# Kernel tuning notes

Hardware: AMD Instinct MI355X
Metric: run time of the kernel (lower is better)

The kernel has to match this reference:

```python
import jax, jax.numpy as jnp
import numpy as np

N, H, B = 500000, 256, 512  # nodes, hidden_dim, number of graphs


def setup_inputs() -> dict:
    key = jax.random.key(0)
    k1, k2, k3, k4 = jax.random.split(key, 4)
    x = jax.random.normal(k1, (N, H), dtype=jnp.float32)
    batch = jnp.sort(jax.random.randint(k2, (N,), 0, B)).astype(jnp.int64)
    # attention_pool params (Linear(H,H) -> Tanh -> Linear(H,1))
    s1 = 1.0 / np.sqrt(H)
    W1 = jax.random.uniform(k3, (H, H), jnp.float32, -s1, s1)
    b1 = jnp.zeros((H,), jnp.float32)
    W2 = jax.random.uniform(k4, (H, 1), jnp.float32, -s1, s1)
    b2 = jnp.zeros((1,), jnp.float32)
    return {"x": x, "batch": batch, "W1": W1, "b1": b1, "W2": W2, "b2": b2}


def reference(x, batch, W1, b1, W2, b2):
    # attention scores per node: Linear -> tanh -> Linear -> scalar
    s = (jnp.tanh(x @ W1 + b1) @ W2 + b2)[:, 0]            # [N]
    # segment-wise softmax over nodes of each graph (numerically stable)
    seg_max = jax.ops.segment_max(s, batch, num_segments=B)  # [B]
    e = jnp.exp(s - seg_max[batch])                          # [N]
    denom = jax.ops.segment_sum(e, batch, num_segments=B)    # [B]
    w = e / denom[batch]                                     # [N]
    attn_pool = jax.ops.segment_sum(x * w[:, None], batch, num_segments=B)  # [B,H]
    # mean pool
    sums = jax.ops.segment_sum(x, batch, num_segments=B)     # [B,H]
    counts = jax.ops.segment_sum(jnp.ones((x.shape[0],), x.dtype), batch, num_segments=B)
    mean_pool = sums / jnp.maximum(counts, 1.0)[:, None]
    # max pool (guard empty segments -> 0, matching zero-init buffer behavior)
    max_pool = jax.ops.segment_max(x, batch, num_segments=B)
    max_pool = jnp.where(counts[:, None] > 0, max_pool, 0.0)
    return jnp.concatenate([mean_pool, max_pool, attn_pool], axis=1)  # [B, 3H]
```

## Files before the change

### kernel.cpp

```cpp
#include <hip/hip_runtime.h>

#define HDIM 256
#define MTILE 64
#define NITER 4
#define APITCH 264
#define PROWS 256
#define CHUNK 16

typedef __attribute__((ext_vector_type(8))) short short8;
typedef __attribute__((ext_vector_type(4))) short short4v;
typedef __attribute__((ext_vector_type(4))) float floatx4;

__device__ __forceinline__ unsigned short f2bf(float f){
  unsigned u = __float_as_uint(f);
  u += 0x7FFFu + ((u>>16)&1u);
  return (unsigned short)(u>>16);
}
__device__ __forceinline__ unsigned fkey(float f){
  unsigned u = __float_as_uint(f);
  return u ^ ((unsigned)((int)u>>31) | 0x80000000u);
}
__device__ __forceinline__ float fdec(unsigned u){
  unsigned b = (u & 0x80000000u) ? (u & 0x7FFFFFFFu) : ~u;
  return __uint_as_float(b);
}

__global__ void k_zero(float* __restrict__ p, int n){
  int i = blockIdx.x*256 + threadIdx.x;
  if (i < n) p[i] = 0.f;
}

__global__ void k_prep(const float* __restrict__ w1, unsigned short* __restrict__ w1t){
  int col = blockIdx.x, k = threadIdx.x;
  w1t[col*HDIM + k] = f2bf(w1[k*HDIM + col]);
}

__global__ void k_bounds(const int* __restrict__ batch, int* __restrict__ segstart,
                         int n, int B){
  int i = blockIdx.x*256 + threadIdx.x;
  if (i >= n) return;
  int b = batch[i];
  int prev = (i == 0) ? -1 : batch[i-1];
  if (prev != b) for (int q = prev+1; q <= b; ++q) segstart[q] = i;
  if (i == n-1) for (int q = b+1; q <= B; ++q) segstart[q] = n;
}

__launch_bounds__(256)
__global__ void k_scores(const float* __restrict__ x,
                         const unsigned short* __restrict__ w1t,
                         const float* __restrict__ b1,
                         const float* __restrict__ w2,
                         const float* __restrict__ b2,
                         float* __restrict__ s, int n)
{
  __shared__ unsigned short As[MTILE*APITCH];
  __shared__ float sp[4][MTILE];
  const int t = threadIdx.x;
  const int wv = t>>6;
  const int lane = t&63;
  const int l15 = lane&15;
  const int quad = lane>>4;
  const long long base = (long long)blockIdx.x * (MTILE*NITER);

  short8 bf[8][4];
  float b1v[4], w2v[4];
  const int cb = wv*64;
  #pragma unroll
  for (int ct=0; ct<4; ++ct){
    int col = cb + ct*16 + l15;
    b1v[ct] = b1[col];
    w2v[ct] = w2[col];
    #pragma unroll
    for (int kc=0; kc<8; ++kc)
      bf[kc][ct] = *(const short8*)(w1t + (size_t)col*HDIM + kc*32 + quad*8);
  }

  const float4* x4 = (const float4*)x;
  for (int it = 0; it < NITER; ++it){
    const long long node0 = base + (long long)it*MTILE;
    if (node0 >= n) break;

    #pragma unroll
    for (int j=0; j<MTILE/4; ++j){
      int f = j*256 + t;
      int row = f>>6, c4 = f&63;
      long long gr = node0 + row;
      float4 v = make_float4(0.f,0.f,0.f,0.f);
      if (gr < n) v = x4[gr*(HDIM/4) + c4];
      short4v p;
      p.x=(short)f2bf(v.x); p.y=(short)f2bf(v.y); p.z=(short)f2bf(v.z); p.w=(short)f2bf(v.w);
      *(short4v*)(As + row*APITCH + c4*4) = p;
    }
    __syncthreads();

    #pragma unroll 1
    for (int rt=0; rt<MTILE/16; ++rt){
      floatx4 acc[4];
      #pragma unroll
      for (int ct=0;ct<4;++ct) acc[ct] = (floatx4){0.f,0.f,0.f,0.f};
      #pragma unroll
      for (int kc=0; kc<8; ++kc){
        short8 a = *(const short8*)(As + (rt*16 + l15)*APITCH + kc*32 + quad*8);
        #pragma unroll
        for (int ct=0; ct<4; ++ct)
          acc[ct] = __builtin_amdgcn_mfma_f32_16x16x32_bf16(a, bf[kc][ct], acc[ct], 0, 0, 0);
      }
      float part[4] = {0.f,0.f,0.f,0.f};
      #pragma unroll
      for (int ct=0; ct<4; ++ct){
        #pragma unroll
        for (int r=0; r<4; ++r){
          float h = acc[ct][r] + b1v[ct];
          float z = fminf(fmaxf(2.f*h, -30.f), 30.f);
          float e = __expf(z);
          part[r] += __fdividef(e-1.f, e+1.f) * w2v[ct];
        }
      }
      #pragma unroll
      for (int off=8; off>=1; off>>=1){
        #pragma unroll
        for (int r=0;r<4;++r) part[r] += __shfl_xor(part[r], off, 64);
      }
      if (l15==0){
        #pragma unroll
        for (int r=0;r<4;++r) sp[wv][rt*16 + quad*4 + r] = part[r];
      }
    }
    __syncthreads();
    if (t < MTILE){
      long long gr = node0 + t;
      if (gr < n) s[gr] = sp[0][t]+sp[1][t]+sp[2][t]+sp[3][t] + b2[0];
    }
  }
}

__global__ void k_seg(float* __restrict__ s, const int* __restrict__ segstart,
                      float* __restrict__ denom, float* __restrict__ counts){
  __shared__ float red[4];
  const int b = blockIdx.x;
  const int t = threadIdx.x;
  const int lane = t&63, wv = t>>6;
  const int start = segstart[b], end = segstart[b+1];

  float m = -INFINITY;
  for (int i = start + t; i < end; i += 256) m = fmaxf(m, s[i]);
  #pragma unroll
  for (int off=32; off>=1; off>>=1) m = fmaxf(m, __shfl_xor(m, off, 64));
  if (lane==0) red[wv] = m;
  __syncthreads();
  m = fmaxf(fmaxf(red[0],red[1]), fmaxf(red[2],red[3]));

  float acc = 0.f;
  for (int i = start + t; i < end; i += 256){
    float e = __expf(s[i] - m);
    s[i] = e; acc += e;
  }
  #pragma unroll
  for (int off=32; off>=1; off>>=1) acc += __shfl_xor(acc, off, 64);
  __syncthreads();
  if (lane==0) red[wv] = acc;
  __syncthreads();
  if (t==0){
    float total = red[0]+red[1]+red[2]+red[3];
    denom[b] = (total > 0.f) ? total : 1.f;
    counts[b] = (float)(end - start);
  }
}

__launch_bounds__(256)
__global__ void k_pool(const float* __restrict__ x, const int* __restrict__ batch,
                       const float* __restrict__ e, const float* __restrict__ denom,
                       float* __restrict__ sums, unsigned* __restrict__ maxu,
                       float* __restrict__ attn, int n){
  const int t = threadIdx.x;
  long long r0 = (long long)blockIdx.x * PROWS;
  if (r0 >= n) return;
  long long r1 = r0 + PROWS; if (r1 > n) r1 = n;
  int curb = batch[r0];
  float rd = 1.f/denom[curb];
  float sum=0.f, att=0.f, mx=-INFINITY;
  long long i = r0;
  while (i < r1){
    if (i + CHUNK <= r1 && batch[i + CHUNK - 1] == curb){
      float v[CHUNK], w[CHUNK];
      #pragma unroll
      for (int k=0;k<CHUNK;++k) v[k] = x[(i+k)*HDIM + t];
      #pragma unroll
      for (int k=0;k<CHUNK;++k) w[k] = e[i+k];
      #pragma unroll
      for (int k=0;k<CHUNK;++k){
        sum += v[k];
        att += v[k]*(w[k]*rd);
        mx = fmaxf(mx, v[k]);
      }
      i += CHUNK;
    } else {
      int b = batch[i];
      if (b != curb){
        atomicAdd(&sums[(size_t)curb*HDIM + t], sum);
        atomicAdd(&attn[(size_t)curb*HDIM + t], att);
        atomicMax(&maxu[(size_t)curb*HDIM + t], fkey(mx));
        curb=b; rd = 1.f/denom[b]; sum=0.f; att=0.f; mx=-INFINITY;
      }
      float v = x[i*HDIM + t];
      sum += v; att += v*(e[i]*rd); mx = fmaxf(mx, v);
      ++i;
    }
  }
  atomicAdd(&sums[(size_t)curb*HDIM + t], sum);
  atomicAdd(&attn[(size_t)curb*HDIM + t], att);
  atomicMax(&maxu[(size_t)curb*HDIM + t], fkey(mx));
}

__global__ void k_fin(const float* __restrict__ sums, const unsigned* __restrict__ maxu,
                      const float* __restrict__ attn, const float* __restrict__ counts,
                      float* __restrict__ out, int bcount){
  int idx = blockIdx.x*256 + threadIdx.x;
  int total = bcount*3*HDIM;
  if (idx >= total) return;
  int b = idx / (3*HDIM);
  int c = idx - b*(3*HDIM);
  float cnt = counts[b];
  float v;
  if (c < HDIM)        v = sums[(size_t)b*HDIM + c] / fmaxf(cnt, 1.f);
  else if (c < 2*HDIM) v = (cnt > 0.f) ? fdec(maxu[(size_t)b*HDIM + (c-HDIM)]) : 0.f;
  else                 v = attn[(size_t)b*HDIM + (c-2*HDIM)];
  out[idx] = v;
}

extern "C" void kernel_launch(void* const* d_in, const int* in_sizes, int n_in,
                              void* d_out, int out_size, void* d_ws, size_t ws_size,
                              hipStream_t stream){
  const float* x   = (const float*)d_in[0];
  const int* batch = (const int*)d_in[1];
  const float* W1  = (const float*)d_in[2];
  const float* b1  = (const float*)d_in[3];
  const float* W2  = (const float*)d_in[4];
  const float* b2  = (const float*)d_in[5];
  float* out = (float*)d_out;
  const int n = in_sizes[1];
  const int B = out_size / (3*HDIM);

  char* w = (char*)d_ws;
  unsigned short* W1T = (unsigned short*)w;
  size_t off = (size_t)HDIM*HDIM*2;
  float* s = (float*)(w + off);
  off += (size_t)((n+3)&~3)*4;
  int* segstart = (int*)(w + off);
  off += (size_t)((B+4)&~3)*4;
  float* stats = (float*)(w + off);
  float* denom  = stats;
  float* counts = stats + B;
  float* sums   = stats + 2*B;
  unsigned* maxu = (unsigned*)(stats + 2*B + (size_t)B*HDIM);
  float* attn   = stats + 2*B + 2*(size_t)B*HDIM;
  int zerowords = 3*B*HDIM;

  hipLaunchKernelGGL(k_zero, dim3((zerowords+255)/256), dim3(256), 0, stream, sums, zerowords);
  hipLaunchKernelGGL(k_prep, dim3(HDIM), dim3(HDIM), 0, stream, W1, W1T);
  hipLaunchKernelGGL(k_bounds, dim3((n+255)/256), dim3(256), 0, stream, batch, segstart, n, B);
  hipLaunchKernelGGL(k_scores, dim3((n + MTILE*NITER - 1)/(MTILE*NITER)), dim3(256), 0, stream,
                     x, W1T, b1, W2, b2, s, n);
  hipLaunchKernelGGL(k_seg, dim3(B), dim3(256), 0, stream, s, segstart, denom, counts);
  hipLaunchKernelGGL(k_pool, dim3((n+PROWS-1)/PROWS), dim3(256), 0, stream,
                     x, batch, s, denom, sums, maxu, attn, n);
  hipLaunchKernelGGL(k_fin, dim3((out_size+255)/256), dim3(256), 0, stream,
                     sums, maxu, attn, counts, out, B);
}
```

Baseline: 899.6 us.

## Emit bf16 copy of x in score kernel and pool from it

The score kernel already converts each x tile to bf16 for the MFMA matmul. It now also writes that bf16 tile to a workspace buffer. The pooling kernel reads this half-width copy, with two columns per thread and two rows per step, instead of re-reading fp32 x. The aim is to halve the pooling kernel's read traffic. The cost is an extra 256 MB write in the score kernel. Mean, max and attention pools are now computed from bf16-rounded inputs, which may break accuracy tolerance, especially for max pool. Pool row and chunk sizes are also doubled.

Result: no change. 909.4 us (+1.1%).

```diff
diff --git a/kernel.cpp b/kernel.cpp
--- a/kernel.cpp
+++ b/kernel.cpp
@@ -4,8 +4,8 @@
 #define MTILE 64
 #define NITER 4
 #define APITCH 264
-#define PROWS 256
-#define CHUNK 16
+#define PROWS 512
+#define CHUNK 32
 
 typedef __attribute__((ext_vector_type(8))) short short8;
 typedef __attribute__((ext_vector_type(4))) short short4v;
@@ -15,6 +15,9 @@
   unsigned u = __float_as_uint(f);
   u += 0x7FFFu + ((u>>16)&1u);
   return (unsigned short)(u>>16);
+}
+__device__ __forceinline__ float bf2f(unsigned short h){
+  return __uint_as_float(((unsigned)h)<<16);
 }
 __device__ __forceinline__ unsigned fkey(float f){
   unsigned u = __float_as_uint(f);
@@ -51,7 +54,8 @@
                          const float* __restrict__ b1,
                          const float* __restrict__ w2,
                          const float* __restrict__ b2,
-                         float* __restrict__ s, int n)
+                         float* __restrict__ s,
+                         unsigned short* __restrict__ xbf, int n)
 {
   __shared__ unsigned short As[MTILE*APITCH];
   __shared__ float sp[4][MTILE];
@@ -90,6 +94,7 @@
       short4v p;
       p.x=(short)f2bf(v.x); p.y=(short)f2bf(v.y); p.z=(short)f2bf(v.z); p.w=(short)f2bf(v.w);
       *(short4v*)(As + row*APITCH + c4*4) = p;
+      if (gr < n) *(short4v*)(xbf + gr*HDIM + c4*4) = p;
     }
     __syncthreads();
 
@@ -168,48 +173,64 @@
 }
 
 __launch_bounds__(256)
-__global__ void k_pool(const float* __restrict__ x, const int* __restrict__ batch,
+__global__ void k_pool(const unsigned short* __restrict__ xbf, const int* __restrict__ batch,
                        const float* __restrict__ e, const float* __restrict__ denom,
                        float* __restrict__ sums, unsigned* __restrict__ maxu,
                        float* __restrict__ attn, int n){
   const int t = threadIdx.x;
+  const int col = (t&127)*2;
+  const int ro = t>>7;
   long long r0 = (long long)blockIdx.x * PROWS;
   if (r0 >= n) return;
   long long r1 = r0 + PROWS; if (r1 > n) r1 = n;
+
   int curb = batch[r0];
   float rd = 1.f/denom[curb];
-  float sum=0.f, att=0.f, mx=-INFINITY;
+  float s0=0.f,s1=0.f,a0=0.f,a1=0.f,m0=-INFINITY,m1=-INFINITY;
+
   long long i = r0;
   while (i < r1){
     if (i + CHUNK <= r1 && batch[i + CHUNK - 1] == curb){
-      float v[CHUNK], w[CHUNK];
-      #pragma unroll
-      for (int k=0;k<CHUNK;++k) v[k] = x[(i+k)*HDIM + t];
-      #pragma unroll
-      for (int k=0;k<CHUNK;++k) w[k] = e[i+k];
-      #pragma unroll
-      for (int k=0;k<CHUNK;++k){
-        sum += v[k];
-        att += v[k]*(w[k]*rd);
-        mx = fmaxf(mx, v[k]);
+      #pragma unroll
+      for (int k=0;k<CHUNK/2;++k){
+        long long row = i + 2*k + ro;
+        unsigned u = *(const unsigned*)(xbf + row*HDIM + col);
+        float w = e[row]*rd;
+        float v0 = bf2f((unsigned short)(u & 0xFFFFu));
+        float v1 = bf2f((unsigned short)(u >> 16));
+        s0 += v0; s1 += v1; a0 += v0*w; a1 += v1*w;
+        m0 = fmaxf(m0, v0); m1 = fmaxf(m1, v1);
       }
       i += CHUNK;
     } else {
-      int b = batch[i];
-      if (b != curb){
-        atomicAdd(&sums[(size_t)curb*HDIM + t], sum);
-        atomicAdd(&attn[(size_t)curb*HDIM + t], att);
-        atomicMax(&maxu[(size_t)curb*HDIM + t], fkey(mx));
-        curb=b; rd = 1.f/denom[b]; sum=0.f; att=0.f; mx=-INFINITY;
-      }
-      float v = x[i*HDIM + t];
-      sum += v; att += v*(e[i]*rd); mx = fmaxf(mx, v);
-      ++i;
-    }
-  }
-  atomicAdd(&sums[(size_t)curb*HDIM + t], sum);
-  atomicAdd(&attn[(size_t)curb*HDIM + t], att);
-  atomicMax(&maxu[(size_t)curb*HDIM + t], fkey(mx));
+      long long row = i + ro;
+      if (row < r1){
+        int b = batch[row];
+        if (b != curb){
+          atomicAdd(&sums[(size_t)curb*HDIM + col],   s0);
+          atomicAdd(&sums[(size_t)curb*HDIM + col+1], s1);
+          atomicAdd(&attn[(size_t)curb*HDIM + col],   a0);
+          atomicAdd(&attn[(size_t)curb*HDIM + col+1], a1);
+          if (m0 > -INFINITY) atomicMax(&maxu[(size_t)curb*HDIM + col],   fkey(m0));
+          if (m1 > -INFINITY) atomicMax(&maxu[(size_t)curb*HDIM + col+1], fkey(m1));
+          curb=b; rd=1.f/denom[b]; s0=s1=a0=a1=0.f; m0=m1=-INFINITY;
+        }
+        unsigned u = *(const unsigned*)(xbf + row*HDIM + col);
+        float w = e[row]*rd;
+        float v0 = bf2f((unsigned short)(u & 0xFFFFu));
+        float v1 = bf2f((unsigned short)(u >> 16));
+        s0 += v0; s1 += v1; a0 += v0*w; a1 += v1*w;
+        m0 = fmaxf(m0, v0); m1 = fmaxf(m1, v1);
+      }
+      i += 2;
+    }
+  }
+  atomicAdd(&sums[(size_t)curb*HDIM + col],   s0);
+  atomicAdd(&sums[(size_t)curb*HDIM + col+1], s1);
+  atomicAdd(&attn[(size_t)curb*HDIM + col],   a0);
+  atomicAdd(&attn[(size_t)curb*HDIM + col+1], a1);
+  if (m0 > -INFINITY) atomicMax(&maxu[(size_t)curb*HDIM + col],   fkey(m0));
+  if (m1 > -INFINITY) atomicMax(&maxu[(size_t)curb*HDIM + col+1], fkey(m1));
 }
 
 __global__ void k_fin(const float* __restrict__ sums, const unsigned* __restrict__ maxu,
@@ -242,8 +263,10 @@
   const int B = out_size / (3*HDIM);
 
   char* w = (char*)d_ws;
-  unsigned short* W1T = (unsigned short*)w;
-  size_t off = (size_t)HDIM*HDIM*2;
+  unsigned short* xbf = (unsigned short*)w;
+  size_t off = ((size_t)n*HDIM*2 + 255) & ~(size_t)255;
+  unsigned short* W1T = (unsigned short*)(w + off);
+  off += (size_t)HDIM*HDIM*2;
   float* s = (float*)(w + off);
   off += (size_t)((n+3)&~3)*4;
   int* segstart = (int*)(w + off);
@@ -260,10 +283,10 @@
   hipLaunchKernelGGL(k_prep, dim3(HDIM), dim3(HDIM), 0, stream, W1, W1T);
   hipLaunchKernelGGL(k_bounds, dim3((n+255)/256), dim3(256), 0, stream, batch, segstart, n, B);
   hipLaunchKernelGGL(k_scores, dim3((n + MTILE*NITER - 1)/(MTILE*NITER)), dim3(256), 0, stream,
-                     x, W1T, b1, W2, b2, s, n);
+                     x, W1T, b1, W2, b2, s, xbf, n);
   hipLaunchKernelGGL(k_seg, dim3(B), dim3(256), 0, stream, s, segstart, denom, counts);
-  hipLaunchKernelGGL(k_pool, dim3((n+PROWS-1)/PROWS), dim3(256), 0, stream,
-                     x, batch, s, denom, sums, maxu, attn, n);
+  hipLaunchKernelGGL(k_pool, dim3((int)((n+PROWS-1)/PROWS)), dim3(256), 0, stream,
+                     xbf, batch, s, denom, sums, maxu, attn, n);
   hipLaunchKernelGGL(k_fin, dim3((out_size+255)/256), dim3(256), 0, stream,
                      sums, maxu, attn, counts, out, B);
 }
```
